# Performance work log

Measured on AMD Instinct MI355X. Metric: run time of the kernel, lower is better.

Reference implementation:

```python
import jax, jax.numpy as jnp
import numpy as np

N_NODES = 100000
C = 128
E = 800000
V = 50000
NEG_SLOPE = 0.2


def gat_conv(x, edges, W, att_src, att_dst, bias, num_nodes):
    """Single-head PyG-style GATConv with self-loops added (PyG default).

    edges: [2, E] with row 0 = source j, row 1 = destination i.
    """
    loops = jnp.arange(num_nodes, dtype=edges.dtype)
    src = jnp.concatenate([edges[0], loops])  # [E+N]
    dst = jnp.concatenate([edges[1], loops])

    h = x @ W.T                               # [N, C] linear transform
    a_s = h @ att_src                         # [N] per-node src score
    a_d = h @ att_dst                         # [N] per-node dst score

    e = jax.nn.leaky_relu(a_s[src] + a_d[dst], NEG_SLOPE)  # [E+N]
    # scatter-softmax over edges grouped by destination node
    m = jax.ops.segment_max(e, dst, num_segments=num_nodes)
    ex = jnp.exp(e - m[dst])
    denom = jax.ops.segment_sum(ex, dst, num_segments=num_nodes)
    alpha = ex / (denom[dst] + 1e-16)         # [E+N]

    out = jax.ops.segment_sum(alpha[:, None] * h[src], dst, num_segments=num_nodes)
    return out + bias


def setup_inputs() -> dict:
    key = jax.random.key(0)
    ks = jax.random.split(key, 12)
    s = 1.0 / np.sqrt(C)
    return {
        "embedding": jax.random.normal(ks[0], (N_NODES, C), jnp.float32),
        "W1": jax.random.normal(ks[1], (C, C), jnp.float32) * s,
        "att_src1": jax.random.normal(ks[2], (C,), jnp.float32) * s,
        "att_dst1": jax.random.normal(ks[3], (C,), jnp.float32) * s,
        "b1": jax.random.normal(ks[4], (C,), jnp.float32) * s,
        "W2": jax.random.normal(ks[5], (C, C), jnp.float32) * s,
        "att_src2": jax.random.normal(ks[6], (C,), jnp.float32) * s,
        "att_dst2": jax.random.normal(ks[7], (C,), jnp.float32) * s,
        "b2": jax.random.normal(ks[8], (C,), jnp.float32) * s,
        "edges1": jax.random.randint(ks[9], (2, E), 0, N_NODES, jnp.int64 if jax.config.jax_enable_x64 else jnp.int32),
        "edges2": jax.random.randint(ks[10], (2, E), 0, N_NODES, jnp.int64 if jax.config.jax_enable_x64 else jnp.int32),
        "idx_mapping": jax.random.randint(ks[11], (V,), 0, N_NODES, jnp.int64 if jax.config.jax_enable_x64 else jnp.int32),
    }


def reference(embedding, W1, att_src1, att_dst1, b1, W2, att_src2, att_dst2, b2,
              edges1, edges2, idx_mapping):
    h = gat_conv(embedding, edges1, W1, att_src1, att_dst1, b1, N_NODES)
    h = gat_conv(h, edges2, W2, att_src2, att_dst2, b2, N_NODES)
    return h[idx_mapping]
```

## Files before the change

kernel.cpp:

```cpp
#include <hip/hip_runtime.h>

#define N_NODES 100000
#define C_DIM 128
#define E_EDGES 800000
#define V_OUT 50000
#define EN (E_EDGES + N_NODES)
#define M2 (2 * N_NODES)
#define EN2 (2 * EN)

#define BSHIFT 9
#define NBUCK_L ((N_NODES + 511) >> 9)
#define NBUCK2 (2 * NBUCK_L)
#define CAP 8192
#define P1_CHUNK 4096
#define P1_PER_T (P1_CHUNK / 256)
#define NCHUNK ((EN2 + P1_CHUNK - 1) / P1_CHUNK)

#define XPAD 136
#define LDS_E 768

typedef unsigned int uint;
typedef unsigned short ushort;
typedef __attribute__((ext_vector_type(8))) short bf16x8;
typedef __attribute__((ext_vector_type(4))) float f32x4;

static __device__ __forceinline__ ushort f2bf(float f) {
    uint u = __float_as_uint(f);
    u += 0x7fffu + ((u >> 16) & 1);
    return (ushort)(u >> 16);
}

#define PREP_WBLK (C_DIM * C_DIM / 4 / 256)
#define PREP_VBLK ((V_OUT + 255) / 256)
__global__ void prep_kernel(const float* __restrict__ W1, const float* __restrict__ W2,
                            ushort* __restrict__ W1b, ushort* __restrict__ W2b,
                            const int* __restrict__ idx, int* __restrict__ vflag)
{
    const int b = blockIdx.x;
    if (b < 2 * PREP_WBLK) {
        const float* in  = (b < PREP_WBLK) ? W1 : W2;
        ushort* outp     = (b < PREP_WBLK) ? W1b : W2b;
        int i = (b % PREP_WBLK) * 256 + threadIdx.x;
        float4 v = reinterpret_cast<const float4*>(in)[i];
        ushort4 r;
        r.x = f2bf(v.x); r.y = f2bf(v.y); r.z = f2bf(v.z); r.w = f2bf(v.w);
        reinterpret_cast<ushort4*>(outp)[i] = r;
    } else {
        int v = (b - 2 * PREP_WBLK) * 256 + threadIdx.x;
        if (v < V_OUT) vflag[idx[v]] = 1;
    }
}

template <int IN_F32>
__global__ __launch_bounds__(256) void gemm_mfma(
    const void* __restrict__ xin, const ushort* __restrict__ Wb,
    const float* __restrict__ att_s, const float* __restrict__ att_d,
    ushort* __restrict__ hb, float* __restrict__ a_s, float* __restrict__ a_d)
{
    __shared__ ushort xs[64 * XPAD];
    __shared__ ushort ws[128 * XPAD];
    const int tid = threadIdx.x;
    const int nb = blockIdx.x * 64;

    {
        const int row = tid >> 2, q = tid & 3;
        const long srow = min(nb + row, N_NODES - 1);
        ushort* dst = &xs[row * XPAD + q * 32];
        if (IN_F32) {
            const float* src = (const float*)xin + srow * 128 + q * 32;
            #pragma unroll
            for (int i = 0; i < 4; ++i) {
                float4 u = *reinterpret_cast<const float4*>(src + i * 8);
                float4 v = *reinterpret_cast<const float4*>(src + i * 8 + 4);
                uint4 pk;
                pk.x = (uint)f2bf(u.x) | ((uint)f2bf(u.y) << 16);
                pk.y = (uint)f2bf(u.z) | ((uint)f2bf(u.w) << 16);
                pk.z = (uint)f2bf(v.x) | ((uint)f2bf(v.y) << 16);
                pk.w = (uint)f2bf(v.z) | ((uint)f2bf(v.w) << 16);
                *reinterpret_cast<uint4*>(dst + i * 8) = pk;
            }
        } else {
            const ushort* src = (const ushort*)xin + srow * 128 + q * 32;
            #pragma unroll
            for (int i = 0; i < 4; ++i)
                *reinterpret_cast<uint4*>(dst + i * 8) =
                    *reinterpret_cast<const uint4*>(src + i * 8);
        }
    }
    {
        const int row = tid >> 1, half = tid & 1;
        const ushort* src = Wb + row * 128 + half * 64;
        ushort* dst = &ws[row * XPAD + half * 64];
        #pragma unroll
        for (int i = 0; i < 8; ++i)
            *reinterpret_cast<uint4*>(dst + i * 8) =
                *reinterpret_cast<const uint4*>(src + i * 8);
    }
    __syncthreads();

    const int lane = tid & 63;
    const int wv   = tid >> 6;
    const int n0   = nb + wv * 16;
    if (n0 >= N_NODES) return;
    const int m    = lane & 15;
    const int quad = lane >> 4;

    bf16x8 a[4];
    #pragma unroll
    for (int ki = 0; ki < 4; ++ki)
        a[ki] = *reinterpret_cast<const bf16x8*>(&xs[(wv * 16 + m) * XPAD + quad * 8 + ki * 32]);

    float ps[4] = {0, 0, 0, 0}, pd[4] = {0, 0, 0, 0};

    #pragma unroll
    for (int ct = 0; ct < 8; ++ct) {
        const int c = ct * 16 + m;
        f32x4 acc = {0.f, 0.f, 0.f, 0.f};
        #pragma unroll
        for (int ki = 0; ki < 4; ++ki) {
            bf16x8 b = *reinterpret_cast<const bf16x8*>(&ws[c * XPAD + quad * 8 + ki * 32]);
            acc = __builtin_amdgcn_mfma_f32_16x16x32_bf16(a[ki], b, acc, 0, 0, 0);
        }
        const float asc = att_s[c], adc = att_d[c];
        #pragma unroll
        for (int r = 0; r < 4; ++r) {
            const int node = n0 + quad * 4 + r;
            hb[(long)node * 128 + c] = f2bf(acc[r]);
            ps[r] = fmaf(acc[r], asc, ps[r]);
            pd[r] = fmaf(acc[r], adc, pd[r]);
        }
    }
    #pragma unroll
    for (int r = 0; r < 4; ++r) {
        float s = ps[r], d = pd[r];
        #pragma unroll
        for (int x = 1; x < 16; x <<= 1) { s += __shfl_xor(s, x); d += __shfl_xor(d, x); }
        if (m == 0) {
            const int node = n0 + quad * 4 + r;
            a_s[node] = s; a_d[node] = d;
        }
    }
}

__global__ __launch_bounds__(256) void partition_kernel(
    const int* __restrict__ e1, const int* __restrict__ e2,
    int* __restrict__ cursor, uint* __restrict__ slab)
{
    __shared__ int cnt[NBUCK2];
    __shared__ int basearr[NBUCK2];
    const int tid = threadIdx.x;
    for (int i = tid; i < NBUCK2; i += 256) cnt[i] = 0;
    __syncthreads();

    const int e0 = blockIdx.x * P1_CHUNK;
    uint ent[P1_PER_T];
    int  bkt[P1_PER_T];
    #pragma unroll
    for (int i = 0; i < P1_PER_T; ++i) {
        int e = e0 + i * 256 + tid;
        bkt[i] = -1;
        if (e < EN2) {
            int src, dst, lb;
            if (e < EN) {
                if (e < E_EDGES) { src = e1[e]; dst = e1[E_EDGES + e]; }
                else             { src = dst = e - E_EDGES; }
                lb = 0;
            } else {
                int f = e - EN;
                if (f < E_EDGES) { src = e2[f]; dst = e2[E_EDGES + f]; }
                else             { src = dst = f - E_EDGES; }
                lb = NBUCK_L;
            }
            bkt[i] = lb + (dst >> BSHIFT);
            ent[i] = (uint)src | ((uint)(dst & 511) << 17);
            atomicAdd(&cnt[bkt[i]], 1);
        }
    }
    __syncthreads();
    for (int b = tid; b < NBUCK2; b += 256) {
        int c = cnt[b];
        basearr[b] = (c > 0) ? atomicAdd(&cursor[b], c) : 0;
        cnt[b] = 0;
    }
    __syncthreads();
    #pragma unroll
    for (int i = 0; i < P1_PER_T; ++i) {
        if (bkt[i] >= 0) {
            int r = basearr[bkt[i]] + atomicAdd(&cnt[bkt[i]], 1);
            if (r < CAP) slab[(long)bkt[i] * CAP + r] = ent[i];
        }
    }
}

__global__ __launch_bounds__(256) void local_csr(
    const uint* __restrict__ slab, const int* __restrict__ cursor,
    int* __restrict__ offs, uint* __restrict__ esrc)
{
    __shared__ uint ent[CAP];
    __shared__ int deg[512];
    __shared__ int excl[512];
    __shared__ int sbase;
    const int b = blockIdx.x;
    const int tid = threadIdx.x;
    const int cnt = min(cursor[b], CAP);
    const int layer = (b >= NBUCK_L);
    const int node0 = (b - layer * NBUCK_L) << BSHIFT;
    const int obase = layer * N_NODES;
    const int nodes_n = min(512, N_NODES - node0);

    for (int i = tid; i < 512; i += 256) deg[i] = 0;
    if (tid < 64) {
        int s = 0;
        #pragma unroll
        for (int k = 0; k < 7; ++k) {
            int idx = tid + 64 * k;
            if (idx < b) s += cursor[idx];
        }
        #pragma unroll
        for (int d = 32; d > 0; d >>= 1) s += __shfl_down(s, d);
        if (tid == 0) sbase = s;
    }
    __syncthreads();
    const int base = sbase;

    for (int i = tid; i < cnt; i += 256) {
        uint v = slab[(long)b * CAP + i];
        ent[i] = v;
        atomicAdd(&deg[v >> 17], 1);
    }
    __syncthreads();
    if (tid < 64) {
        int v8[8]; int s = 0;
        #pragma unroll
        for (int i = 0; i < 8; ++i) { v8[i] = deg[tid * 8 + i]; s += v8[i]; }
        int incl = s;
        #pragma unroll
        for (int d = 1; d < 64; d <<= 1) {
            int t = __shfl_up(incl, d);
            if (tid >= d) incl += t;
        }
        int e = incl - s;
        #pragma unroll
        for (int i = 0; i < 8; ++i) { excl[tid * 8 + i] = e; e += v8[i]; }
    }
    __syncthreads();
    for (int i = tid; i < nodes_n; i += 256)
        offs[obase + node0 + i] = base + excl[i];
    for (int i = tid; i < 512; i += 256) deg[i] = 0;
    if (tid == 0 && node0 + 512 >= N_NODES)
        offs[obase + N_NODES] = base + cnt;
    __syncthreads();
    for (int i = tid; i < cnt; i += 256) {
        uint v = ent[i];
        int dl = v >> 17;
        int r = atomicAdd(&deg[dl], 1);
        esrc[base + excl[dl] + r] = v;
    }
}

template <int MODE>
__global__ __launch_bounds__(256) void aggregate(
    const ushort* __restrict__ hb, const float* __restrict__ a_s,
    const float* __restrict__ a_d, const float* __restrict__ bias,
    const int* __restrict__ offs, const uint* __restrict__ esrc,
    const int* __restrict__ vflag, void* __restrict__ outp, int obase)
{
    __shared__ uint2 ew[LDS_E];
    const int tid = threadIdx.x;
    const int node0 = blockIdx.x * 16;
    const int bnode0 = (node0 >> BSHIFT) << BSHIFT;
    const int bstart = offs[obase + node0];
    const int bend   = offs[obase + node0 + 16];
    const int nE = bend - bstart;

    for (int i = tid; i < min(nE, LDS_E); i += 256) {
        uint v = esrc[bstart + i];
        float w = 0.0f;
        const int d = bnode0 + (v >> 17);
        if (MODE == 0 || vflag[d] != 0) {
            float e = a_s[v & 0x1ffff] + a_d[d];
            e = (e >= 0.0f) ? e : 0.2f * e;
            w = __expf(e);
        }
        ew[i] = make_uint2(v, __float_as_uint(w));
    }
    __syncthreads();

    const int wave = tid >> 6;
    const int lane = tid & 63;
    const int slot = lane >> 4;
    const int c16  = lane & 15;
    const int node = node0 + wave * 4 + slot;
    if (MODE == 1 && vflag[node] == 0) return;

    const int start = offs[obase + node];
    const int end   = offs[obase + node + 1];
    const long coff = (long)(c16 << 3);
    float acc[8] = {0, 0, 0, 0, 0, 0, 0, 0};
    float dsum = 0.0f;

    if (start < end) {
        if (nE <= LDS_E) {
            const int jr = start - bstart, jend = end - bstart;
            const int e1 = jend - 1;
            uint2 p0 = ew[jr];
            uint2 p1 = ew[min(jr + 1, e1)];
            uint2 p2 = ew[min(jr + 2, e1)];
            uint2 p3 = ew[min(jr + 3, e1)];
            uint4 h0 = *reinterpret_cast<const uint4*>(hb + ((long)(p0.x & 0x1ffff) << 7) + coff);
            uint4 h1 = *reinterpret_cast<const uint4*>(hb + ((long)(p1.x & 0x1ffff) << 7) + coff);
            uint4 h2 = *reinterpret_cast<const uint4*>(hb + ((long)(p2.x & 0x1ffff) << 7) + coff);
            uint4 h3 = *reinterpret_cast<const uint4*>(hb + ((long)(p3.x & 0x1ffff) << 7) + coff);
            float w0 = __uint_as_float(p0.y);
            float w1 = __uint_as_float(p1.y);
            float w2 = __uint_as_float(p2.y);
            float w3 = __uint_as_float(p3.y);
            for (int j = jr; j < jend; ++j) {
                uint2 p4 = ew[min(j + 4, e1)];
                uint4 h4 = *reinterpret_cast<const uint4*>(hb + ((long)(p4.x & 0x1ffff) << 7) + coff);
                float w4 = __uint_as_float(p4.y);
                dsum += w0;
                acc[0] = fmaf(w0, __uint_as_float(h0.x << 16),         acc[0]);
                acc[1] = fmaf(w0, __uint_as_float(h0.x & 0xffff0000u), acc[1]);
                acc[2] = fmaf(w0, __uint_as_float(h0.y << 16),         acc[2]);
                acc[3] = fmaf(w0, __uint_as_float(h0.y & 0xffff0000u), acc[3]);
                acc[4] = fmaf(w0, __uint_as_float(h0.z << 16),         acc[4]);
                acc[5] = fmaf(w0, __uint_as_float(h0.z & 0xffff0000u), acc[5]);
                acc[6] = fmaf(w0, __uint_as_float(h0.w << 16),         acc[6]);
                acc[7] = fmaf(w0, __uint_as_float(h0.w & 0xffff0000u), acc[7]);
                w0 = w1; w1 = w2; w2 = w3; w3 = w4;
                h0 = h1; h1 = h2; h2 = h3; h3 = h4;
            }
        } else {
            const float ad = a_d[node];
            for (int j = start; j < end; ++j) {
                uint v = esrc[j];
                float e = a_s[v & 0x1ffff] + ad;
                e = (e >= 0.0f) ? e : 0.2f * e;
                float w = __expf(e);
                uint4 h = *reinterpret_cast<const uint4*>(hb + ((long)(v & 0x1ffff) << 7) + coff);
                dsum += w;
                acc[0] = fmaf(w, __uint_as_float(h.x << 16),         acc[0]);
                acc[1] = fmaf(w, __uint_as_float(h.x & 0xffff0000u), acc[1]);
                acc[2] = fmaf(w, __uint_as_float(h.y << 16),         acc[2]);
                acc[3] = fmaf(w, __uint_as_float(h.y & 0xffff0000u), acc[3]);
                acc[4] = fmaf(w, __uint_as_float(h.z << 16),         acc[4]);
                acc[5] = fmaf(w, __uint_as_float(h.z & 0xffff0000u), acc[5]);
                acc[6] = fmaf(w, __uint_as_float(h.w << 16),         acc[6]);
                acc[7] = fmaf(w, __uint_as_float(h.w & 0xffff0000u), acc[7]);
            }
        }
    }

    const float inv = 1.0f / (dsum + 1e-16f);
    const int c0 = c16 << 3;
    const float4 b0 = *reinterpret_cast<const float4*>(bias + c0);
    const float4 b1 = *reinterpret_cast<const float4*>(bias + c0 + 4);
    float res[8];
    res[0] = fmaf(acc[0], inv, b0.x);
    res[1] = fmaf(acc[1], inv, b0.y);
    res[2] = fmaf(acc[2], inv, b0.z);
    res[3] = fmaf(acc[3], inv, b0.w);
    res[4] = fmaf(acc[4], inv, b1.x);
    res[5] = fmaf(acc[5], inv, b1.y);
    res[6] = fmaf(acc[6], inv, b1.z);
    res[7] = fmaf(acc[7], inv, b1.w);
    if (MODE == 0) {
        uint4 pk;
        pk.x = (uint)f2bf(res[0]) | ((uint)f2bf(res[1]) << 16);
        pk.y = (uint)f2bf(res[2]) | ((uint)f2bf(res[3]) << 16);
        pk.z = (uint)f2bf(res[4]) | ((uint)f2bf(res[5]) << 16);
        pk.w = (uint)f2bf(res[6]) | ((uint)f2bf(res[7]) << 16);
        *reinterpret_cast<uint4*>((ushort*)outp + ((long)node << 7) + c0) = pk;
    } else {
        float* op = (float*)outp + ((long)node << 7) + c0;
        *reinterpret_cast<float4*>(op)     = make_float4(res[0], res[1], res[2], res[3]);
        *reinterpret_cast<float4*>(op + 4) = make_float4(res[4], res[5], res[6], res[7]);
    }
}

__global__ void gather_out(const float* __restrict__ h, const int* __restrict__ idx,
                           float* __restrict__ out)
{
    int g = blockIdx.x * 256 + threadIdx.x;
    int v = g >> 5, c4 = (g & 31) << 2;
    long src = (long)idx[v] * C_DIM + c4;
    *reinterpret_cast<float4*>(out + ((long)v * C_DIM + c4)) =
        *reinterpret_cast<const float4*>(h + src);
}

extern "C" void kernel_launch(void* const* d_in, const int* in_sizes, int n_in,
                              void* d_out, int out_size, void* d_ws, size_t ws_size,
                              hipStream_t stream)
{
    const float* emb = (const float*)d_in[0];
    const float* W1  = (const float*)d_in[1];
    const float* as1 = (const float*)d_in[2];
    const float* ad1 = (const float*)d_in[3];
    const float* b1  = (const float*)d_in[4];
    const float* W2  = (const float*)d_in[5];
    const float* as2 = (const float*)d_in[6];
    const float* ad2 = (const float*)d_in[7];
    const float* b2  = (const float*)d_in[8];
    const int* edges1 = (const int*)d_in[9];
    const int* edges2 = (const int*)d_in[10];
    const int* idxm   = (const int*)d_in[11];
    float* out = (float*)d_out;

    char* p = (char*)d_ws;
    auto alloc = [&](size_t bytes) {
        char* r = p;
        p += (bytes + 255) & ~(size_t)255;
        return r;
    };
    float*  hB   = (float*)alloc((size_t)N_NODES * C_DIM * 4);
    ushort* hb   = (ushort*)alloc((size_t)N_NODES * C_DIM * 2);
    ushort* a1o  = (ushort*)alloc((size_t)N_NODES * C_DIM * 2);
    uint*   slab = (uint*)alloc((size_t)NBUCK2 * CAP * 4);
    uint*   esrc = (uint*)alloc((size_t)EN2 * 4);
    int*    offs = (int*)alloc((size_t)(M2 + 1) * 4);
    ushort* W1b  = (ushort*)alloc((size_t)C_DIM * C_DIM * 2);
    ushort* W2b  = (ushort*)alloc((size_t)C_DIM * C_DIM * 2);
    float*  aS   = (float*)alloc((size_t)N_NODES * 4);
    float*  aD   = (float*)alloc((size_t)N_NODES * 4);
    int*  cursor = (int*)alloc((size_t)NBUCK2 * 4);
    int*  vflag  = (int*)alloc((size_t)N_NODES * 4);

    hipMemsetAsync(cursor, 0, (size_t)((char*)vflag - (char*)cursor) + (size_t)N_NODES * 4, stream);
    prep_kernel<<<2 * PREP_WBLK + PREP_VBLK, 256, 0, stream>>>(W1, W2, W1b, W2b, idxm, vflag);

    partition_kernel<<<NCHUNK, 256, 0, stream>>>(edges1, edges2, cursor, slab);
    local_csr<<<NBUCK2, 256, 0, stream>>>(slab, cursor, offs, esrc);

    gemm_mfma<1><<<(N_NODES + 63) / 64, 256, 0, stream>>>(emb, W1b, as1, ad1, hb, aS, aD);
    aggregate<0><<<N_NODES / 16, 256, 0, stream>>>(hb, aS, aD, b1, offs, esrc, vflag, a1o, 0);

    gemm_mfma<0><<<(N_NODES + 63) / 64, 256, 0, stream>>>(a1o, W2b, as2, ad2, hb, aS, aD);
    aggregate<1><<<N_NODES / 16, 256, 0, stream>>>(hb, aS, aD, b2, offs, esrc, vflag, hB, N_NODES);

    gather_out<<<(V_OUT * 32) / 256, 256, 0, stream>>>(hB, idxm, out);
}
```

Measured before the change: 271.0 us.

## Make GEMM persistent with double-buffered prefetch and staged coalesced output

The GEMM becomes a persistent kernel with a fixed grid of 512 blocks. Each block converts W from fp32 to bf16 once into LDS, then loops over 64-row chunks, prefetching the next chunk into registers and a second LDS buffer while computing the current one. Output rows are staged through LDS so they are written to global memory as 16-byte coalesced stores instead of scattered 2-byte stores. The separate prep kernel is removed: W conversion moves into the GEMM and the vflag marking moves into extra partition blocks. This saves a launch and the scattered writes, at the cost of more LDS, extra barriers and per-block W conversion.

```diff
diff --git a/kernel.cpp b/kernel.cpp
--- a/kernel.cpp
+++ b/kernel.cpp
@@ -15,9 +15,13 @@
 #define P1_CHUNK 4096
 #define P1_PER_T (P1_CHUNK / 256)
 #define NCHUNK ((EN2 + P1_CHUNK - 1) / P1_CHUNK)
+#define VFLAG_BLKS ((V_OUT + 255) / 256)
 
 #define XPAD 136
 #define LDS_E 768
+
+#define NCHUNKS_G ((N_NODES + 63) / 64)
+#define GEMM_GRID 512
 
 typedef unsigned int uint;
 typedef unsigned short ushort;
@@ -30,129 +34,181 @@
     return (ushort)(u >> 16);
 }
 
-#define PREP_WBLK (C_DIM * C_DIM / 4 / 256)
-#define PREP_VBLK ((V_OUT + 255) / 256)
-__global__ void prep_kernel(const float* __restrict__ W1, const float* __restrict__ W2,
-                            ushort* __restrict__ W1b, ushort* __restrict__ W2b,
-                            const int* __restrict__ idx, int* __restrict__ vflag)
-{
-    const int b = blockIdx.x;
-    if (b < 2 * PREP_WBLK) {
-        const float* in  = (b < PREP_WBLK) ? W1 : W2;
-        ushort* outp     = (b < PREP_WBLK) ? W1b : W2b;
-        int i = (b % PREP_WBLK) * 256 + threadIdx.x;
-        float4 v = reinterpret_cast<const float4*>(in)[i];
-        ushort4 r;
-        r.x = f2bf(v.x); r.y = f2bf(v.y); r.z = f2bf(v.z); r.w = f2bf(v.w);
-        reinterpret_cast<ushort4*>(outp)[i] = r;
-    } else {
-        int v = (b - 2 * PREP_WBLK) * 256 + threadIdx.x;
-        if (v < V_OUT) vflag[idx[v]] = 1;
-    }
-}
-
 template <int IN_F32>
 __global__ __launch_bounds__(256) void gemm_mfma(
-    const void* __restrict__ xin, const ushort* __restrict__ Wb,
+    const void* __restrict__ xin, const float* __restrict__ W,
     const float* __restrict__ att_s, const float* __restrict__ att_d,
     ushort* __restrict__ hb, float* __restrict__ a_s, float* __restrict__ a_d)
 {
-    __shared__ ushort xs[64 * XPAD];
     __shared__ ushort ws[128 * XPAD];
+    __shared__ ushort xs[2][64 * XPAD];
     const int tid = threadIdx.x;
-    const int nb = blockIdx.x * 64;
 
     {
-        const int row = tid >> 2, q = tid & 3;
-        const long srow = min(nb + row, N_NODES - 1);
-        ushort* dst = &xs[row * XPAD + q * 32];
+        const int row = tid >> 1, half = tid & 1;
+        const float* src = W + row * 128 + half * 64;
+        ushort* dst = &ws[row * XPAD + half * 64];
+        #pragma unroll
+        for (int i = 0; i < 8; ++i) {
+            float4 u = *reinterpret_cast<const float4*>(src + i * 8);
+            float4 v = *reinterpret_cast<const float4*>(src + i * 8 + 4);
+            uint4 pk;
+            pk.x = (uint)f2bf(u.x) | ((uint)f2bf(u.y) << 16);
+            pk.y = (uint)f2bf(u.z) | ((uint)f2bf(u.w) << 16);
+            pk.z = (uint)f2bf(v.x) | ((uint)f2bf(v.y) << 16);
+            pk.w = (uint)f2bf(v.z) | ((uint)f2bf(v.w) << 16);
+            *reinterpret_cast<uint4*>(dst + i * 8) = pk;
+        }
+    }
+
+    const int srow_t = tid >> 2, q = tid & 3;
+    const int lane = tid & 63, wv = tid >> 6;
+    const int m = lane & 15, quad = lane >> 4;
+
+    int c = blockIdx.x;
+    float4 pf_f[8];
+    uint4  pf_b[4];
+
+    {
+        const long srow = min((long)c * 64 + srow_t, (long)N_NODES - 1);
         if (IN_F32) {
             const float* src = (const float*)xin + srow * 128 + q * 32;
             #pragma unroll
-            for (int i = 0; i < 4; ++i) {
-                float4 u = *reinterpret_cast<const float4*>(src + i * 8);
-                float4 v = *reinterpret_cast<const float4*>(src + i * 8 + 4);
-                uint4 pk;
-                pk.x = (uint)f2bf(u.x) | ((uint)f2bf(u.y) << 16);
-                pk.y = (uint)f2bf(u.z) | ((uint)f2bf(u.w) << 16);
-                pk.z = (uint)f2bf(v.x) | ((uint)f2bf(v.y) << 16);
-                pk.w = (uint)f2bf(v.z) | ((uint)f2bf(v.w) << 16);
-                *reinterpret_cast<uint4*>(dst + i * 8) = pk;
-            }
+            for (int i = 0; i < 8; ++i)
+                pf_f[i] = *reinterpret_cast<const float4*>(src + i * 4);
         } else {
             const ushort* src = (const ushort*)xin + srow * 128 + q * 32;
             #pragma unroll
             for (int i = 0; i < 4; ++i)
-                *reinterpret_cast<uint4*>(dst + i * 8) =
-                    *reinterpret_cast<const uint4*>(src + i * 8);
-        }
-    }
-    {
-        const int row = tid >> 1, half = tid & 1;
-        const ushort* src = Wb + row * 128 + half * 64;
-        ushort* dst = &ws[row * XPAD + half * 64];
-        #pragma unroll
-        for (int i = 0; i < 8; ++i)
-            *reinterpret_cast<uint4*>(dst + i * 8) =
-                *reinterpret_cast<const uint4*>(src + i * 8);
-    }
-    __syncthreads();
-
-    const int lane = tid & 63;
-    const int wv   = tid >> 6;
-    const int n0   = nb + wv * 16;
-    if (n0 >= N_NODES) return;
-    const int m    = lane & 15;
-    const int quad = lane >> 4;
-
-    bf16x8 a[4];
-    #pragma unroll
-    for (int ki = 0; ki < 4; ++ki)
-        a[ki] = *reinterpret_cast<const bf16x8*>(&xs[(wv * 16 + m) * XPAD + quad * 8 + ki * 32]);
-
-    float ps[4] = {0, 0, 0, 0}, pd[4] = {0, 0, 0, 0};
-
-    #pragma unroll
-    for (int ct = 0; ct < 8; ++ct) {
-        const int c = ct * 16 + m;
-        f32x4 acc = {0.f, 0.f, 0.f, 0.f};
-        #pragma unroll
-        for (int ki = 0; ki < 4; ++ki) {
-            bf16x8 b = *reinterpret_cast<const bf16x8*>(&ws[c * XPAD + quad * 8 + ki * 32]);
-            acc = __builtin_amdgcn_mfma_f32_16x16x32_bf16(a[ki], b, acc, 0, 0, 0);
-        }
-        const float asc = att_s[c], adc = att_d[c];
+                pf_b[i] = *reinterpret_cast<const uint4*>(src + i * 8);
+        }
+        ushort* dst = &xs[0][srow_t * XPAD + q * 32];
+        if (IN_F32) {
+            #pragma unroll
+            for (int i = 0; i < 4; ++i) {
+                uint4 pk;
+                pk.x = (uint)f2bf(pf_f[2*i].x)   | ((uint)f2bf(pf_f[2*i].y)   << 16);
+                pk.y = (uint)f2bf(pf_f[2*i].z)   | ((uint)f2bf(pf_f[2*i].w)   << 16);
+                pk.z = (uint)f2bf(pf_f[2*i+1].x) | ((uint)f2bf(pf_f[2*i+1].y) << 16);
+                pk.w = (uint)f2bf(pf_f[2*i+1].z) | ((uint)f2bf(pf_f[2*i+1].w) << 16);
+                *reinterpret_cast<uint4*>(dst + i * 8) = pk;
+            }
+        } else {
+            #pragma unroll
+            for (int i = 0; i < 4; ++i)
+                *reinterpret_cast<uint4*>(dst + i * 8) = pf_b[i];
+        }
+    }
+    __syncthreads();
+
+    int cur = 0;
+    while (c < NCHUNKS_G) {
+        const int cn = c + GEMM_GRID;
+
+        if (cn < NCHUNKS_G) {
+            const long srow = min((long)cn * 64 + srow_t, (long)N_NODES - 1);
+            if (IN_F32) {
+                const float* src = (const float*)xin + srow * 128 + q * 32;
+                #pragma unroll
+                for (int i = 0; i < 8; ++i)
+                    pf_f[i] = *reinterpret_cast<const float4*>(src + i * 4);
+            } else {
+                const ushort* src = (const ushort*)xin + srow * 128 + q * 32;
+                #pragma unroll
+                for (int i = 0; i < 4; ++i)
+                    pf_b[i] = *reinterpret_cast<const uint4*>(src + i * 8);
+            }
+        }
+
+        const int n0 = c * 64 + wv * 16;
+        bf16x8 a[4];
+        #pragma unroll
+        for (int ki = 0; ki < 4; ++ki)
+            a[ki] = *reinterpret_cast<const bf16x8*>(&xs[cur][(wv*16+m)*XPAD + quad*8 + ki*32]);
+        __syncthreads();
+
+        float ps[4] = {0, 0, 0, 0}, pd[4] = {0, 0, 0, 0};
+        #pragma unroll
+        for (int ct = 0; ct < 8; ++ct) {
+            const int cc = ct * 16 + m;
+            f32x4 acc = {0.f, 0.f, 0.f, 0.f};
+            #pragma unroll
+            for (int ki = 0; ki < 4; ++ki) {
+                bf16x8 b = *reinterpret_cast<const bf16x8*>(&ws[cc*XPAD + quad*8 + ki*32]);
+                acc = __builtin_amdgcn_mfma_f32_16x16x32_bf16(a[ki], b, acc, 0, 0, 0);
+            }
+            const float asc = att_s[cc], adc = att_d[cc];
+            #pragma unroll
+            for (int r = 0; r < 4; ++r) {
+                xs[cur][(wv*16 + quad*4 + r) * XPAD + cc] = f2bf(acc[r]);
+                ps[r] = fmaf(acc[r], asc, ps[r]);
+                pd[r] = fmaf(acc[r], adc, pd[r]);
+            }
+        }
+        __syncthreads();
+
+        {
+            const int sub = tid & 15, rb = tid >> 4;
+            #pragma unroll
+            for (int i = 0; i < 4; ++i) {
+                const int rl = rb + i * 16;
+                const int node = c * 64 + rl;
+                uint4 v = *reinterpret_cast<const uint4*>(&xs[cur][rl * XPAD + sub * 8]);
+                if (node < N_NODES)
+                    *reinterpret_cast<uint4*>(hb + (long)node * 128 + sub * 8) = v;
+            }
+        }
         #pragma unroll
         for (int r = 0; r < 4; ++r) {
+            float s = ps[r], d = pd[r];
+            #pragma unroll
+            for (int x = 1; x < 16; x <<= 1) { s += __shfl_xor(s, x); d += __shfl_xor(d, x); }
             const int node = n0 + quad * 4 + r;
-            hb[(long)node * 128 + c] = f2bf(acc[r]);
-            ps[r] = fmaf(acc[r], asc, ps[r]);
-            pd[r] = fmaf(acc[r], adc, pd[r]);
-        }
-    }
-    #pragma unroll
-    for (int r = 0; r < 4; ++r) {
-        float s = ps[r], d = pd[r];
-        #pragma unroll
-        for (int x = 1; x < 16; x <<= 1) { s += __shfl_xor(s, x); d += __shfl_xor(d, x); }
-        if (m == 0) {
-            const int node = n0 + quad * 4 + r;
-            a_s[node] = s; a_d[node] = d;
-        }
+            if (m == 0 && node < N_NODES) { a_s[node] = s; a_d[node] = d; }
+        }
+
+        if (cn < NCHUNKS_G) {
+            ushort* dst = &xs[cur ^ 1][srow_t * XPAD + q * 32];
+            if (IN_F32) {
+                #pragma unroll
+                for (int i = 0; i < 4; ++i) {
+                    uint4 pk;
+                    pk.x = (uint)f2bf(pf_f[2*i].x)   | ((uint)f2bf(pf_f[2*i].y)   << 16);
+                    pk.y = (uint)f2bf(pf_f[2*i].z)   | ((uint)f2bf(pf_f[2*i].w)   << 16);
+                    pk.z = (uint)f2bf(pf_f[2*i+1].x) | ((uint)f2bf(pf_f[2*i+1].y) << 16);
+                    pk.w = (uint)f2bf(pf_f[2*i+1].z) | ((uint)f2bf(pf_f[2*i+1].w) << 16);
+                    *reinterpret_cast<uint4*>(dst + i * 8) = pk;
+                }
+            } else {
+                #pragma unroll
+                for (int i = 0; i < 4; ++i)
+                    *reinterpret_cast<uint4*>(dst + i * 8) = pf_b[i];
+            }
+        }
+        __syncthreads();
+        cur ^= 1;
+        c = cn;
     }
 }
 
 __global__ __launch_bounds__(256) void partition_kernel(
     const int* __restrict__ e1, const int* __restrict__ e2,
-    int* __restrict__ cursor, uint* __restrict__ slab)
+    int* __restrict__ cursor, uint* __restrict__ slab,
+    const int* __restrict__ idxm, int* __restrict__ vflag)
 {
     __shared__ int cnt[NBUCK2];
     __shared__ int basearr[NBUCK2];
     const int tid = threadIdx.x;
+    const int blk = blockIdx.x;
+    if (blk >= NCHUNK) {
+        int v = (blk - NCHUNK) * 256 + tid;
+        if (v < V_OUT) vflag[idxm[v]] = 1;
+        return;
+    }
     for (int i = tid; i < NBUCK2; i += 256) cnt[i] = 0;
     __syncthreads();
 
-    const int e0 = blockIdx.x * P1_CHUNK;
+    const int e0 = blk * P1_CHUNK;
     uint ent[P1_PER_T];
     int  bkt[P1_PER_T];
     #pragma unroll
@@ -419,23 +475,21 @@
     uint*   slab = (uint*)alloc((size_t)NBUCK2 * CAP * 4);
     uint*   esrc = (uint*)alloc((size_t)EN2 * 4);
     int*    offs = (int*)alloc((size_t)(M2 + 1) * 4);
-    ushort* W1b  = (ushort*)alloc((size_t)C_DIM * C_DIM * 2);
-    ushort* W2b  = (ushort*)alloc((size_t)C_DIM * C_DIM * 2);
     float*  aS   = (float*)alloc((size_t)N_NODES * 4);
     float*  aD   = (float*)alloc((size_t)N_NODES * 4);
     int*  cursor = (int*)alloc((size_t)NBUCK2 * 4);
     int*  vflag  = (int*)alloc((size_t)N_NODES * 4);
 
     hipMemsetAsync(cursor, 0, (size_t)((char*)vflag - (char*)cursor) + (size_t)N_NODES * 4, stream);
-    prep_kernel<<<2 * PREP_WBLK + PREP_VBLK, 256, 0, stream>>>(W1, W2, W1b, W2b, idxm, vflag);
-
-    partition_kernel<<<NCHUNK, 256, 0, stream>>>(edges1, edges2, cursor, slab);
+
+    partition_kernel<<<NCHUNK + VFLAG_BLKS, 256, 0, stream>>>(
+        edges1, edges2, cursor, slab, idxm, vflag);
     local_csr<<<NBUCK2, 256, 0, stream>>>(slab, cursor, offs, esrc);
 
-    gemm_mfma<1><<<(N_NODES + 63) / 64, 256, 0, stream>>>(emb, W1b, as1, ad1, hb, aS, aD);
+    gemm_mfma<1><<<GEMM_GRID, 256, 0, stream>>>(emb, W1, as1, ad1, hb, aS, aD);
     aggregate<0><<<N_NODES / 16, 256, 0, stream>>>(hb, aS, aD, b1, offs, esrc, vflag, a1o, 0);
 
-    gemm_mfma<0><<<(N_NODES + 63) / 64, 256, 0, stream>>>(a1o, W2b, as2, ad2, hb, aS, aD);
+    gemm_mfma<0><<<GEMM_GRID, 256, 0, stream>>>(a1o, W2, as2, ad2, hb, aS, aD);
     aggregate<1><<<N_NODES / 16, 256, 0, stream>>>(hb, aS, aD, b2, offs, esrc, vflag, hB, N_NODES);
 
     gather_out<<<(V_OUT * 32) / 256, 256, 0, stream>>>(hB, idxm, out);
```

Result: no change. 275.1 us (+1.5%).
